# Optimization experiments

Hardware: AMD Instinct MI355X
Metric: run time of the kernel (lower is better)

The kernel has to match this reference:

```python
import jax, jax.numpy as jnp
import numpy as np

NUM_HEADS = 16
HEAD_DIM = 80
HIDDEN = 1280
SEQ = 3072
NUM_SEGS = 6  # 6 packed images of 512 patches each


def rotate_half(x):
    x1, x2 = jnp.split(x, 2, axis=-1)
    return jnp.concatenate([-x2, x1], axis=-1)


def setup_inputs() -> dict:
    key = jax.random.key(0)
    ks = jax.random.split(key, 6)
    hidden_states = jax.random.normal(ks[0], (SEQ, HIDDEN), dtype=jnp.float32)
    # RoPE tables as in Qwen-VL vision: freqs over half the head_dim, duplicated
    half = HEAD_DIM // 2
    inv_freq = 1.0 / (10000.0 ** (jnp.arange(half, dtype=jnp.float32) / half))
    pos = jnp.arange(SEQ, dtype=jnp.float32)[:, None]
    freqs = pos * inv_freq[None, :]                      # (SEQ, half)
    emb = jnp.concatenate([freqs, freqs], axis=-1)       # (SEQ, HEAD_DIM)
    cos = jnp.cos(emb)
    sin = jnp.sin(emb)
    # Packed segment boundaries: [0, 512, 1024, ..., 3072]
    cu_seqlens = jnp.arange(0, SEQ + 1, SEQ // NUM_SEGS, dtype=jnp.int32)
    scale = 0.02
    w_qkv = jax.random.normal(ks[1], (3 * HIDDEN, HIDDEN), dtype=jnp.float32) * scale
    b_qkv = jax.random.normal(ks[2], (3 * HIDDEN,), dtype=jnp.float32) * scale
    w_proj = jax.random.normal(ks[3], (HIDDEN, HIDDEN), dtype=jnp.float32) * scale
    b_proj = jax.random.normal(ks[4], (HIDDEN,), dtype=jnp.float32) * scale
    return {
        "hidden_states": hidden_states, "cos": cos, "sin": sin,
        "w_qkv": w_qkv, "b_qkv": b_qkv, "w_proj": w_proj, "b_proj": b_proj,
        "cu_seqlens": cu_seqlens,
    }


def reference(hidden_states, cos, sin, w_qkv, b_qkv, w_proj, b_proj, cu_seqlens):
    S, H = hidden_states.shape
    nh, hd = NUM_HEADS, H // NUM_HEADS

    # Fused QKV projection: (S, 3H) -> q, k, v each (S, nh, hd)
    qkv = hidden_states @ w_qkv.T + b_qkv
    qkv = qkv.reshape(S, 3, nh, hd)
    q, k, v = qkv[:, 0], qkv[:, 1], qkv[:, 2]

    # Inline RoPE on q/k (cos/sin broadcast over heads)
    c = cos[:, None, :]
    s = sin[:, None, :]
    q = q * c + rotate_half(q) * s
    k = k * c + rotate_half(k) * s

    # Original casts fp32 -> fp16 for the flash attention kernel
    q16 = q.astype(jnp.float16)
    k16 = k.astype(jnp.float16)
    v16 = v.astype(jnp.float16)

    # Varlen masking: tokens attend only within their own packed segment
    tok = jnp.arange(S)
    seg = jnp.searchsorted(cu_seqlens, tok, side="right")  # (S,)
    same_seg = seg[:, None] == seg[None, :]                 # (S, S)

    scale = hd ** (-0.5)
    # Scores accumulated in fp32 (as flash attention does internally)
    scores = jnp.einsum("qhd,khd->hqk", q16, k16,
                        preferred_element_type=jnp.float32) * scale
    scores = jnp.where(same_seg[None], scores, jnp.finfo(jnp.float32).min)
    weights = jax.nn.softmax(scores, axis=-1).astype(jnp.float16)  # (nh, S, S)

    attn = jnp.einsum("hqk,khd->qhd", weights, v16)  # (S, nh, hd) fp16
    attn = attn.astype(jnp.float32).reshape(S, H)
    return attn @ w_proj.T + b_proj
```

## Files before the change

kernel.cpp:

```cpp
#include <hip/hip_runtime.h>

typedef _Float16 f16;
typedef _Float16 half8 __attribute__((ext_vector_type(8)));
typedef _Float16 half4 __attribute__((ext_vector_type(4)));
typedef float f32x4 __attribute__((ext_vector_type(4)));

__device__ __forceinline__ void gld_lds16(const void* g, void* l) {
  __builtin_amdgcn_global_load_lds((const __attribute__((address_space(1))) void*)g,
                                   (__attribute__((address_space(3))) void*)l, 16, 0, 0);
}

template <int CTRL>
__device__ __forceinline__ float dppf(float x) {
  return __builtin_bit_cast(float,
      __builtin_amdgcn_mov_dpp(__builtin_bit_cast(int, x), CTRL, 0xf, 0xf, true));
}
__device__ __forceinline__ float dpp_max16(float v) {
  v = fmaxf(v, dppf<0xB1>(v));
  v = fmaxf(v, dppf<0x4E>(v));
  v = fmaxf(v, dppf<0x128>(v));
  v = fmaxf(v, dppf<0x140>(v));
  return v;
}
__device__ __forceinline__ float dpp_sum16(float v) {
  v += dppf<0xB1>(v);
  v += dppf<0x4E>(v);
  v += dppf<0x128>(v);
  v += dppf<0x140>(v);
  return v;
}

__global__ void cvt_all(const float* __restrict__ hid, const float* __restrict__ wq,
                        const float* __restrict__ wp, f16* __restrict__ hid16,
                        f16* __restrict__ wq16, f16* __restrict__ wp16) {
  int b = blockIdx.x;
  const float* in;
  f16* out;
  int i;
  if (b < 3840) { in = hid; out = hid16; i = b * 256 + threadIdx.x; }
  else if (b < 8640) { in = wq; out = wq16; i = (b - 3840) * 256 + threadIdx.x; }
  else { in = wp; out = wp16; i = (b - 8640) * 256 + threadIdx.x; }
  float4 v = ((const float4*)in)[i];
  half4 o;
  o.x = (f16)v.x; o.y = (f16)v.y; o.z = (f16)v.z; o.w = (f16)v.w;
  ((half4*)out)[i] = o;
}

__global__ __launch_bounds__(512, 2) void gemm256(const f16* __restrict__ A,
                                                  const f16* __restrict__ B,
                                                  const float* __restrict__ bias,
                                                  f16* __restrict__ C) {
  __shared__ f16 S[65536];
  char* Sb = (char*)S;
  const int tid = threadIdx.x, lane = tid & 63, wid = tid >> 6;
  const int lm = lane & 15, q4 = lane >> 4;
  const int wm = wid >> 2, wn = wid & 3;
  const int bm = blockIdx.x * 256, bn = blockIdx.y * 256;
  const int w2 = wid * 2048;

  const int ch = ((lane & 7) ^ (lane >> 3)) << 3;
  const int r0 = wid * 16 + (lane >> 3);
  const int r1 = r0 + 8;
  uint32_t aoff[2][2], boff[2][2];
#pragma unroll
  for (int h = 0; h < 2; h++) {
    aoff[h][0] = (uint32_t)((bm + h * 64 + (r0 & 63) + ((r0 >> 6) << 7)) * 1280 + ch);
    aoff[h][1] = (uint32_t)((bm + h * 64 + (r1 & 63) + ((r1 >> 6) << 7)) * 1280 + ch);
    boff[h][0] = (uint32_t)((bn + h * 32 + (r0 & 31) + ((r0 >> 5) << 6)) * 1280 + ch);
    boff[h][1] = (uint32_t)((bn + h * 32 + (r1 & 31) + ((r1 >> 5) << 6)) * 1280 + ch);
  }

  int aro[4][2], bro[2][2];
#pragma unroll
  for (int f = 0; f < 4; f++)
#pragma unroll
    for (int ks = 0; ks < 2; ks++) {
      int row = wm * 64 + f * 16 + lm, colb = ks * 64 + q4 * 16;
      aro[f][ks] = row * 128 + (colb ^ ((row & 7) << 4));
    }
#pragma unroll
  for (int j = 0; j < 2; j++)
#pragma unroll
    for (int ks = 0; ks < 2; ks++) {
      int row = wn * 32 + j * 16 + lm, colb = ks * 64 + q4 * 16;
      bro[j][ks] = row * 128 + (colb ^ ((row & 7) << 4));
    }

  f32x4 acc[8][4] = {};

  {
    char* A0 = Sb;
    char* B0 = Sb + 65536;
    char* A1 = Sb + 32768;
    char* B1 = Sb + 98304;
    gld_lds16(A + aoff[0][0], A0 + w2);
    gld_lds16(A + aoff[0][1], A0 + w2 + 1024);
    gld_lds16(B + boff[1][0], B0 + 16384 + w2);
    gld_lds16(B + boff[1][1], B0 + 16384 + w2 + 1024);
    gld_lds16(A + aoff[1][0], A0 + 16384 + w2);
    gld_lds16(A + aoff[1][1], A0 + 16384 + w2 + 1024);
    gld_lds16(B + boff[0][0], B0 + w2);
    gld_lds16(B + boff[0][1], B0 + w2 + 1024);
    gld_lds16(A + aoff[0][0] + 64, A1 + w2);
    gld_lds16(A + aoff[0][1] + 64, A1 + w2 + 1024);
    gld_lds16(B + boff[1][0] + 64, B1 + 16384 + w2);
    gld_lds16(B + boff[1][1] + 64, B1 + 16384 + w2 + 1024);
    gld_lds16(A + aoff[1][0] + 64, A1 + 16384 + w2);
    gld_lds16(A + aoff[1][1] + 64, A1 + 16384 + w2 + 1024);
    asm volatile("s_waitcnt vmcnt(6)" ::: "memory");
    __builtin_amdgcn_s_barrier();
  }

  constexpr int NT = 20;
  half8 af[4][2], bf[2][2];
  for (int t = 0; t < NT; ++t) {
    const int p = t & 1;
    char* Ab = Sb + p * 32768;
    char* Bb = Sb + 65536 + p * 32768;
    char* Bn = Sb + 65536 + (p ^ 1) * 32768;
    const int k1 = (t + 1 < NT ? t + 1 : NT - 1) * 64;
    const int k2 = (t + 2 < NT ? t + 2 : NT - 1) * 64;

#pragma unroll
    for (int f = 0; f < 4; f++) {
      af[f][0] = *(const half8*)(Ab + aro[f][0]);
      af[f][1] = *(const half8*)(Ab + aro[f][1]);
    }
#pragma unroll
    for (int j = 0; j < 2; j++) {
      bf[j][0] = *(const half8*)(Bb + bro[j][0]);
      bf[j][1] = *(const half8*)(Bb + bro[j][1]);
    }
    gld_lds16(B + boff[0][0] + k1, Bn + w2);
    gld_lds16(B + boff[0][1] + k1, Bn + w2 + 1024);
    __builtin_amdgcn_s_barrier();
    asm volatile("s_waitcnt lgkmcnt(0)" ::: "memory");
    __builtin_amdgcn_sched_barrier(0);
    __builtin_amdgcn_s_setprio(1);
#pragma unroll
    for (int ks = 0; ks < 2; ks++)
#pragma unroll
      for (int f = 0; f < 4; f++)
#pragma unroll
        for (int j = 0; j < 2; j++)
          acc[f][j] =
              __builtin_amdgcn_mfma_f32_16x16x32_f16(af[f][ks], bf[j][ks], acc[f][j], 0, 0, 0);
    __builtin_amdgcn_s_setprio(0);
    __builtin_amdgcn_s_barrier();

#pragma unroll
    for (int j = 0; j < 2; j++) {
      bf[j][0] = *(const half8*)(Bb + 16384 + bro[j][0]);
      bf[j][1] = *(const half8*)(Bb + 16384 + bro[j][1]);
    }
    gld_lds16(A + aoff[0][0] + k2, Ab + w2);
    gld_lds16(A + aoff[0][1] + k2, Ab + w2 + 1024);
    __builtin_amdgcn_s_barrier();
    asm volatile("s_waitcnt lgkmcnt(0)" ::: "memory");
    __builtin_amdgcn_sched_barrier(0);
    __builtin_amdgcn_s_setprio(1);
#pragma unroll
    for (int ks = 0; ks < 2; ks++)
#pragma unroll
      for (int f = 0; f < 4; f++)
#pragma unroll
        for (int j = 0; j < 2; j++)
          acc[f][2 + j] =
              __builtin_amdgcn_mfma_f32_16x16x32_f16(af[f][ks], bf[j][ks], acc[f][2 + j], 0, 0, 0);
    __builtin_amdgcn_s_setprio(0);
    __builtin_amdgcn_s_barrier();

#pragma unroll
    for (int f = 0; f < 4; f++) {
      af[f][0] = *(const half8*)(Ab + 16384 + aro[f][0]);
      af[f][1] = *(const half8*)(Ab + 16384 + aro[f][1]);
    }
    gld_lds16(B + boff[1][0] + k2, Bb + 16384 + w2);
    gld_lds16(B + boff[1][1] + k2, Bb + 16384 + w2 + 1024);
    __builtin_amdgcn_s_barrier();
    asm volatile("s_waitcnt lgkmcnt(0)" ::: "memory");
    __builtin_amdgcn_sched_barrier(0);
    __builtin_amdgcn_s_setprio(1);
#pragma unroll
    for (int ks = 0; ks < 2; ks++)
#pragma unroll
      for (int f = 0; f < 4; f++)
#pragma unroll
        for (int j = 0; j < 2; j++)
          acc[4 + f][2 + j] = __builtin_amdgcn_mfma_f32_16x16x32_f16(af[f][ks], bf[j][ks],
                                                                     acc[4 + f][2 + j], 0, 0, 0);
    __builtin_amdgcn_s_setprio(0);
    __builtin_amdgcn_s_barrier();

#pragma unroll
    for (int j = 0; j < 2; j++) {
      bf[j][0] = *(const half8*)(Bb + bro[j][0]);
      bf[j][1] = *(const half8*)(Bb + bro[j][1]);
    }
    gld_lds16(A + aoff[1][0] + k2, Ab + 16384 + w2);
    gld_lds16(A + aoff[1][1] + k2, Ab + 16384 + w2 + 1024);
    asm volatile("s_waitcnt vmcnt(6)" ::: "memory");
    __builtin_amdgcn_s_barrier();
    asm volatile("s_waitcnt lgkmcnt(0)" ::: "memory");
    __builtin_amdgcn_sched_barrier(0);
    __builtin_amdgcn_s_setprio(1);
#pragma unroll
    for (int ks = 0; ks < 2; ks++)
#pragma unroll
      for (int f = 0; f < 4; f++)
#pragma unroll
        for (int j = 0; j < 2; j++)
          acc[4 + f][j] =
              __builtin_amdgcn_mfma_f32_16x16x32_f16(af[f][ks], bf[j][ks], acc[4 + f][j], 0, 0, 0);
    __builtin_amdgcn_s_setprio(0);
    __builtin_amdgcn_s_barrier();
  }

#pragma unroll
  for (int mf = 0; mf < 8; mf++)
#pragma unroll
    for (int nf = 0; nf < 4; nf++) {
      const int gc = bn + wn * 64 + nf * 16 + lm;
      const float bb = bias[gc];
      const int gr0 = bm + wm * 128 + mf * 16 + q4 * 4;
#pragma unroll
      for (int r = 0; r < 4; r++)
        C[(size_t)(gr0 + r) * 3840 + gc] = (f16)(acc[mf][nf][r] + bb);
    }
}

template <bool OUT_F16>
__global__ __launch_bounds__(256, 2) void gemm_bt64(const f16* __restrict__ A,
                                                    const f16* __restrict__ B,
                                                    const float* __restrict__ bias,
                                                    void* __restrict__ Cout,
                                                    int K, int lda, int ldb, int ldc) {
  __shared__ f16 As[64 * 32];
  __shared__ f16 Bs[128 * 32];
  const int tid = threadIdx.x, lane = tid & 63, wave = tid >> 6;
  const int bm = blockIdx.x * 64, bn = blockIdx.y * 128;
  const int wm = (wave & 1) * 32, wn = (wave >> 1) * 64;
  const int lm = lane & 15, kq = (lane >> 4) * 8;
  const int arow = tid >> 2, acol = (tid & 3) * 8;

  const f16* Ab = A + (size_t)(bm + arow) * lda + acol;
  const f16* Bb = B + (size_t)(bn + arow) * ldb + acol;
  f16* AsW = As + wave * 512;
  f16* BsW = Bs + wave * 512;

  f32x4 acc[2][4] = {};
  for (int k0 = 0; k0 < K; k0 += 32) {
    gld_lds16(Ab + k0, AsW);
    gld_lds16(Bb + k0, BsW);
    gld_lds16(Bb + (size_t)64 * ldb + k0, BsW + 2048);
    __syncthreads();
    half8 af[2], bf[4];
#pragma unroll
    for (int mt = 0; mt < 2; mt++) af[mt] = *(const half8*)&As[(wm + 16 * mt + lm) * 32 + kq];
#pragma unroll
    for (int nt = 0; nt < 4; nt++) bf[nt] = *(const half8*)&Bs[(wn + 16 * nt + lm) * 32 + kq];
#pragma unroll
    for (int mt = 0; mt < 2; mt++)
#pragma unroll
      for (int nt = 0; nt < 4; nt++)
        acc[mt][nt] = __builtin_amdgcn_mfma_f32_16x16x32_f16(af[mt], bf[nt], acc[mt][nt], 0, 0, 0);
    __syncthreads();
  }
  const int q4 = lane >> 4;
#pragma unroll
  for (int mt = 0; mt < 2; mt++)
#pragma unroll
    for (int nt = 0; nt < 4; nt++)
#pragma unroll
      for (int r = 0; r < 4; r++) {
        int gr = bm + wm + 16 * mt + 4 * q4 + r;
        int gc = bn + wn + 16 * nt + lm;
        float v = acc[mt][nt][r] + bias[gc];
        if (OUT_F16)
          ((f16*)Cout)[(size_t)gr * ldc + gc] = (f16)v;
        else
          ((float*)Cout)[(size_t)gr * ldc + gc] = v;
      }
}

__global__ void rope_transpose(f16* __restrict__ qkv, const float* __restrict__ cosb,
                               const float* __restrict__ sinb, f16* __restrict__ vt) {
  __shared__ f16 tile[64][72];
  const int b = blockIdx.x;
  if (b < 1920) {
    int idx = b * 256 + threadIdx.x;
    int c = idx % 5;
    int t = idx / 5;
    int h = t % 16; t /= 16;
    int qk = t & 1;
    int s = t >> 1;
    size_t base = (size_t)s * 3840 + qk * 1280 + h * 80 + c * 8;
    half8 x = *(half8*)&qkv[base];
    half8 y = *(half8*)&qkv[base + 40];
    const float* cp = cosb + s * 80 + c * 8;
    const float* sp = sinb + s * 80 + c * 8;
    half8 ox, oy;
#pragma unroll
    for (int i = 0; i < 8; i++) {
      float cs = cp[i], sn = sp[i];
      float xf = (float)x[i], yf = (float)y[i];
      ox[i] = (f16)(xf * cs - yf * sn);
      oy[i] = (f16)(yf * cs + xf * sn);
    }
    *(half8*)&qkv[base] = ox;
    *(half8*)&qkv[base + 40] = oy;
  } else {
    const int bb = b - 1920;
    const int bs = (bb % 48) * 64;
    const int bd = (bb / 48) * 64;
    const int r = threadIdx.x >> 2, c = (threadIdx.x & 3) * 16;
    *(uint4*)&tile[r][c] = *(const uint4*)&qkv[(size_t)(bs + r) * 3840 + 2560 + bd + c];
    *(uint4*)&tile[r][c + 8] = *(const uint4*)&qkv[(size_t)(bs + r) * 3840 + 2560 + bd + c + 8];
    __syncthreads();
    f16 tmp[16];
#pragma unroll
    for (int i = 0; i < 16; i++) tmp[i] = tile[c + i][r];
    *(uint4*)&vt[(size_t)(bd + r) * 3072 + bs + c] = *(uint4*)&tmp[0];
    *(uint4*)&vt[(size_t)(bd + r) * 3072 + bs + c + 8] = *(uint4*)&tmp[8];
  }
}

__global__ __launch_bounds__(256, 3) void flash_attn6(const f16* __restrict__ qkv,
                                                      const f16* __restrict__ vt,
                                                      f16* __restrict__ attn) {
  __shared__ f16 S[25088];
  const int tid = threadIdx.x, lane = tid & 63, wave = tid >> 6;
  const int lm = lane & 15, q4 = lane >> 4;
  const int h = blockIdx.x, g = blockIdx.z;
  const int qbase = g * 512 + blockIdx.y * 64 + wave * 16;
  f16* P = S + 20480 + wave * 1152;
  const half8 hz = {};

  const f16* qrow = qkv + (size_t)(qbase + lm) * 3840 + h * 80;
  half8 qf[3];
  qf[0] = *(const half8*)(qrow + q4 * 8);
  qf[1] = *(const half8*)(qrow + 32 + q4 * 8);
  qf[2] = (q4 < 2) ? *(const half8*)(qrow + 64 + q4 * 8) : hz;

  const bool isK = wave < 2;
  const f16* gsrc = isK ? qkv : vt;
  const uint32_t gstep = isK ? (uint32_t)(64 * 3840) : 64u;
  const int cbase = (wave & 1) * 5;
  const uint32_t ldsoff = (isK ? 0u : 5120u) + (uint32_t)cbase * 512u;
  uint32_t goff[5];
#pragma unroll
  for (int i = 0; i < 5; i++) {
    int t = (cbase + i) * 1024 + lane * 16;
    if (isK) {
      int row = t / 160, colb = t % 160;
      goff[i] = (uint32_t)((g * 512 + row) * 3840 + 1280 + h * 80 + (colb >> 1));
    } else {
      int vd = t >> 7, vsb = t & 127;
      int vsrc = vsb ^ ((vd & 7) << 4);
      goff[i] = (uint32_t)((h * 80 + vd) * 3072 + g * 512 + (vsrc >> 1));
    }
  }

  f32x4 oacc[5] = {};
  float mprev[4] = {-1e30f, -1e30f, -1e30f, -1e30f};
  float lsum[4] = {0.f, 0.f, 0.f, 0.f};
  const float sc = 0.11180339887498949f * 1.4426950408889634f;

#pragma unroll
  for (int i = 0; i < 5; i++) gld_lds16(gsrc + goff[i], S + ldsoff + i * 512);
  __syncthreads();

  for (int jj = 0; jj < 8; jj++) {
    const int p = jj & 1;
    f16* Kb = S + p * 10240;
    f16* Vb = Kb + 5120;
    if (jj < 7) {
#pragma unroll
      for (int i = 0; i < 5; i++)
        gld_lds16(gsrc + goff[i] + (uint32_t)(jj + 1) * gstep,
                  S + (p ^ 1) * 10240 + ldsoff + i * 512);
    }

    f32x4 sacc[4] = {};
#pragma unroll
    for (int ks = 0; ks < 3; ks++) {
      half8 bk[4];
#pragma unroll
      for (int nt = 0; nt < 4; nt++)
        bk[nt] = (ks < 2 || q4 < 2)
                     ? *(const half8*)&Kb[(16 * nt + lm) * 80 + 32 * ks + q4 * 8]
                     : hz;
#pragma unroll
      for (int nt = 0; nt < 4; nt++)
        sacc[nt] = __builtin_amdgcn_mfma_f32_16x16x32_f16(qf[ks], bk[nt], sacc[nt], 0, 0, 0);
    }

    float mnew[4], alpha[4], rs[4];
#pragma unroll
    for (int r = 0; r < 4; r++) {
      float v = fmaxf(fmaxf(sacc[0][r], sacc[1][r]), fmaxf(sacc[2][r], sacc[3][r]));
      v = dpp_max16(v);
      mnew[r] = fmaxf(mprev[r], v * sc);
      alpha[r] = __builtin_exp2f(mprev[r] - mnew[r]);
      mprev[r] = mnew[r];
      rs[r] = 0.f;
    }
#pragma unroll
    for (int nt = 0; nt < 4; nt++)
#pragma unroll
      for (int r = 0; r < 4; r++) {
        float pp = __builtin_exp2f(sacc[nt][r] * sc - mnew[r]);
        sacc[nt][r] = pp;
        rs[r] += pp;
      }
#pragma unroll
    for (int r = 0; r < 4; r++) {
      float v = dpp_sum16(rs[r]);
      lsum[r] = alpha[r] * lsum[r] + v;
#pragma unroll
      for (int nt2 = 0; nt2 < 5; nt2++) oacc[nt2][r] *= alpha[r];
    }

#pragma unroll
    for (int nt = 0; nt < 4; nt++)
#pragma unroll
      for (int r = 0; r < 4; r++)
        P[(4 * q4 + r) * 72 + 16 * nt + lm] = (f16)sacc[nt][r];

#pragma unroll
    for (int ks = 0; ks < 2; ks++) {
      half8 ap = *(const half8*)&P[lm * 72 + ks * 32 + q4 * 8];
      half8 bv[5];
#pragma unroll
      for (int nt2 = 0; nt2 < 5; nt2++) {
        int row = 16 * nt2 + lm;
        bv[nt2] = *(const half8*)&Vb[row * 64 + ((ks * 32 + q4 * 8) ^ ((row & 7) << 3))];
      }
#pragma unroll
      for (int nt2 = 0; nt2 < 5; nt2++)
        oacc[nt2] = __builtin_amdgcn_mfma_f32_16x16x32_f16(ap, bv[nt2], oacc[nt2], 0, 0, 0);
    }

    __syncthreads();
  }

#pragma unroll
  for (int r = 0; r < 4; r++) {
    float inv = 1.0f / lsum[r];
    int s = qbase + 4 * q4 + r;
#pragma unroll
    for (int nt2 = 0; nt2 < 5; nt2++)
      attn[(size_t)s * 1280 + h * 80 + 16 * nt2 + lm] = (f16)(oacc[nt2][r] * inv);
  }
}

extern "C" void kernel_launch(void* const* d_in, const int* in_sizes, int n_in,
                              void* d_out, int out_size, void* d_ws, size_t ws_size,
                              hipStream_t stream) {
  const float* hidden = (const float*)d_in[0];
  const float* cosb   = (const float*)d_in[1];
  const float* sinb   = (const float*)d_in[2];
  const float* w_qkv  = (const float*)d_in[3];
  const float* b_qkv  = (const float*)d_in[4];
  const float* w_proj = (const float*)d_in[5];
  const float* b_proj = (const float*)d_in[6];

  char* ws = (char*)d_ws;
  f16* hidden16 = (f16*)(ws + 0);
  f16* wqkv16   = (f16*)(ws + 7864320);
  f16* wproj16  = (f16*)(ws + 17694720);
  f16* qkv16    = (f16*)(ws + 20971520);
  f16* attn16   = (f16*)(ws + 44564480);
  f16* vt16     = hidden16;

  cvt_all<<<10240, 256, 0, stream>>>(hidden, w_qkv, w_proj, hidden16, wqkv16, wproj16);

  gemm256<<<dim3(12, 15), 512, 0, stream>>>(hidden16, wqkv16, b_qkv, qkv16);

  rope_transpose<<<2880, 256, 0, stream>>>(qkv16, cosb, sinb, vt16);

  flash_attn6<<<dim3(16, 8, 6), 256, 0, stream>>>(qkv16, vt16, attn16);

  gemm_bt64<false><<<dim3(48, 10), 256, 0, stream>>>(attn16, wproj16, b_proj, d_out,
                                                     1280, 1280, 1280, 1280);
}
```

Measured before the change: 194.3 us.

## Retile QKV GEMM to 256x192 blocks over 240 workgroups with swizzled mapping

Replaces the 256x256-tile QKV GEMM (180 blocks) with 256x192 tiles, giving 240 blocks so the grid fills more of the MI355X compute units. It adds a block-index swizzle to improve L2 locality and reworks the LDS layout, warp fragment mapping and the pipelined load schedule to match the new tile shape. The trade-off is a smaller tile with lower arithmetic intensity per block, plus a more intricate load/barrier schedule that could expose latency.

```diff
diff --git a/kernel.cpp b/kernel.cpp
--- a/kernel.cpp
+++ b/kernel.cpp
@@ -46,93 +46,79 @@
   ((half4*)out)[i] = o;
 }
 
-__global__ __launch_bounds__(512, 2) void gemm256(const f16* __restrict__ A,
+__global__ __launch_bounds__(512, 2) void gemm240(const f16* __restrict__ A,
                                                   const f16* __restrict__ B,
                                                   const float* __restrict__ bias,
                                                   f16* __restrict__ C) {
-  __shared__ f16 S[65536];
+  __shared__ f16 S[57344];
   char* Sb = (char*)S;
   const int tid = threadIdx.x, lane = tid & 63, wid = tid >> 6;
   const int lm = lane & 15, q4 = lane >> 4;
   const int wm = wid >> 2, wn = wid & 3;
-  const int bm = blockIdx.x * 256, bn = blockIdx.y * 256;
-  const int w2 = wid * 2048;
+  const int swz = ((int)blockIdx.x & 7) * 30 + ((int)blockIdx.x >> 3);
+  const int bm = (swz % 12) * 256, bn = (swz / 12) * 192;
 
   const int ch = ((lane & 7) ^ (lane >> 3)) << 3;
-  const int r0 = wid * 16 + (lane >> 3);
-  const int r1 = r0 + 8;
-  uint32_t aoff[2][2], boff[2][2];
-#pragma unroll
-  for (int h = 0; h < 2; h++) {
-    aoff[h][0] = (uint32_t)((bm + h * 64 + (r0 & 63) + ((r0 >> 6) << 7)) * 1280 + ch);
-    aoff[h][1] = (uint32_t)((bm + h * 64 + (r1 & 63) + ((r1 >> 6) << 7)) * 1280 + ch);
-    boff[h][0] = (uint32_t)((bn + h * 32 + (r0 & 31) + ((r0 >> 5) << 6)) * 1280 + ch);
-    boff[h][1] = (uint32_t)((bn + h * 32 + (r1 & 31) + ((r1 >> 5) << 6)) * 1280 + ch);
-  }
-
-  int aro[4][2], bro[2][2];
-#pragma unroll
-  for (int f = 0; f < 4; f++)
-#pragma unroll
-    for (int ks = 0; ks < 2; ks++) {
-      int row = wm * 64 + f * 16 + lm, colb = ks * 64 + q4 * 16;
-      aro[f][ks] = row * 128 + (colb ^ ((row & 7) << 4));
-    }
-#pragma unroll
-  for (int j = 0; j < 2; j++)
-#pragma unroll
-    for (int ks = 0; ks < 2; ks++) {
-      int row = wn * 32 + j * 16 + lm, colb = ks * 64 + q4 * 16;
-      bro[j][ks] = row * 128 + (colb ^ ((row & 7) << 4));
-    }
-
-  f32x4 acc[8][4] = {};
+  uint32_t aoff[4], boff[3];
+#pragma unroll
+  for (int q = 0; q < 4; q++)
+    aoff[q] = (uint32_t)((bm + q * 64 + wid * 8 + (lane >> 3)) * 1280 + ch);
+#pragma unroll
+  for (int i = 0; i < 3; i++)
+    boff[i] = (uint32_t)((bn + wid * 24 + i * 8 + (lane >> 3)) * 1280 + ch);
+
+  const int xr = (lm & 7) << 4;
+  int aro[2][2], bro[3][2];
+#pragma unroll
+  for (int f = 0; f < 2; f++)
+#pragma unroll
+    for (int ks = 0; ks < 2; ks++)
+      aro[f][ks] = (wm * 32 + f * 16 + lm) * 128 + ((ks * 64 + q4 * 16) ^ xr);
+#pragma unroll
+  for (int nh = 0; nh < 3; nh++)
+#pragma unroll
+    for (int ks = 0; ks < 2; ks++)
+      bro[nh][ks] = (nh * 64 + wn * 16 + lm) * 128 + ((ks * 64 + q4 * 16) ^ xr);
+
+  f32x4 acc[8][3] = {};
 
   {
-    char* A0 = Sb;
-    char* B0 = Sb + 65536;
-    char* A1 = Sb + 32768;
-    char* B1 = Sb + 98304;
-    gld_lds16(A + aoff[0][0], A0 + w2);
-    gld_lds16(A + aoff[0][1], A0 + w2 + 1024);
-    gld_lds16(B + boff[1][0], B0 + 16384 + w2);
-    gld_lds16(B + boff[1][1], B0 + 16384 + w2 + 1024);
-    gld_lds16(A + aoff[1][0], A0 + 16384 + w2);
-    gld_lds16(A + aoff[1][1], A0 + 16384 + w2 + 1024);
-    gld_lds16(B + boff[0][0], B0 + w2);
-    gld_lds16(B + boff[0][1], B0 + w2 + 1024);
-    gld_lds16(A + aoff[0][0] + 64, A1 + w2);
-    gld_lds16(A + aoff[0][1] + 64, A1 + w2 + 1024);
-    gld_lds16(B + boff[1][0] + 64, B1 + 16384 + w2);
-    gld_lds16(B + boff[1][1] + 64, B1 + 16384 + w2 + 1024);
-    gld_lds16(A + aoff[1][0] + 64, A1 + 16384 + w2);
-    gld_lds16(A + aoff[1][1] + 64, A1 + 16384 + w2 + 1024);
+#pragma unroll
+    for (int q = 0; q < 4; q++)
+      gld_lds16(A + aoff[q], Sb + q * 8192 + wid * 1024);
+#pragma unroll
+    for (int i = 0; i < 3; i++)
+      gld_lds16(B + boff[i], Sb + 65536 + (3 * wid + i) * 1024);
+#pragma unroll
+    for (int i = 0; i < 3; i++)
+      gld_lds16(B + boff[i] + 64, Sb + 65536 + 24576 + (3 * wid + i) * 1024);
+#pragma unroll
+    for (int q = 0; q < 3; q++)
+      gld_lds16(A + aoff[q] + 64, Sb + 32768 + q * 8192 + wid * 1024);
     asm volatile("s_waitcnt vmcnt(6)" ::: "memory");
     __builtin_amdgcn_s_barrier();
   }
 
   constexpr int NT = 20;
-  half8 af[4][2], bf[2][2];
+  half8 af[2][2], bf[3][2];
   for (int t = 0; t < NT; ++t) {
     const int p = t & 1;
     char* Ab = Sb + p * 32768;
-    char* Bb = Sb + 65536 + p * 32768;
-    char* Bn = Sb + 65536 + (p ^ 1) * 32768;
+    char* Bb = Sb + 65536 + p * 24576;
     const int k1 = (t + 1 < NT ? t + 1 : NT - 1) * 64;
     const int k2 = (t + 2 < NT ? t + 2 : NT - 1) * 64;
 
 #pragma unroll
-    for (int f = 0; f < 4; f++) {
+    for (int f = 0; f < 2; f++) {
       af[f][0] = *(const half8*)(Ab + aro[f][0]);
       af[f][1] = *(const half8*)(Ab + aro[f][1]);
     }
 #pragma unroll
-    for (int j = 0; j < 2; j++) {
-      bf[j][0] = *(const half8*)(Bb + bro[j][0]);
-      bf[j][1] = *(const half8*)(Bb + bro[j][1]);
-    }
-    gld_lds16(B + boff[0][0] + k1, Bn + w2);
-    gld_lds16(B + boff[0][1] + k1, Bn + w2 + 1024);
+    for (int nh = 0; nh < 3; nh++) {
+      bf[nh][0] = *(const half8*)(Bb + bro[nh][0]);
+      bf[nh][1] = *(const half8*)(Bb + bro[nh][1]);
+    }
+    gld_lds16(A + aoff[3] + k1, Sb + (p ^ 1) * 32768 + 3 * 8192 + wid * 1024);
     __builtin_amdgcn_s_barrier();
     asm volatile("s_waitcnt lgkmcnt(0)" ::: "memory");
     __builtin_amdgcn_sched_barrier(0);
@@ -140,21 +126,23 @@
 #pragma unroll
     for (int ks = 0; ks < 2; ks++)
 #pragma unroll
-      for (int f = 0; f < 4; f++)
-#pragma unroll
-        for (int j = 0; j < 2; j++)
-          acc[f][j] =
-              __builtin_amdgcn_mfma_f32_16x16x32_f16(af[f][ks], bf[j][ks], acc[f][j], 0, 0, 0);
+      for (int f = 0; f < 2; f++)
+#pragma unroll
+        for (int nh = 0; nh < 3; nh++)
+          acc[f][nh] =
+              __builtin_amdgcn_mfma_f32_16x16x32_f16(af[f][ks], bf[nh][ks], acc[f][nh], 0, 0, 0);
     __builtin_amdgcn_s_setprio(0);
     __builtin_amdgcn_s_barrier();
 
 #pragma unroll
-    for (int j = 0; j < 2; j++) {
-      bf[j][0] = *(const half8*)(Bb + 16384 + bro[j][0]);
-      bf[j][1] = *(const half8*)(Bb + 16384 + bro[j][1]);
-    }
-    gld_lds16(A + aoff[0][0] + k2, Ab + w2);
-    gld_lds16(A + aoff[0][1] + k2, Ab + w2 + 1024);
+    for (int f = 0; f < 2; f++) {
+      af[f][0] = *(const half8*)(Ab + 8192 + aro[f][0]);
+      af[f][1] = *(const half8*)(Ab + 8192 + aro[f][1]);
+    }
+#pragma unroll
+    for (int i = 0; i < 3; i++)
+      gld_lds16(B + boff[i] + k2, Bb + (3 * wid + i) * 1024);
+    gld_lds16(A + aoff[0] + k2, Ab + wid * 1024);
     __builtin_amdgcn_s_barrier();
     asm volatile("s_waitcnt lgkmcnt(0)" ::: "memory");
     __builtin_amdgcn_sched_barrier(0);
@@ -162,21 +150,20 @@
 #pragma unroll
     for (int ks = 0; ks < 2; ks++)
 #pragma unroll
-      for (int f = 0; f < 4; f++)
-#pragma unroll
-        for (int j = 0; j < 2; j++)
-          acc[f][2 + j] =
-              __builtin_amdgcn_mfma_f32_16x16x32_f16(af[f][ks], bf[j][ks], acc[f][2 + j], 0, 0, 0);
+      for (int f = 0; f < 2; f++)
+#pragma unroll
+        for (int nh = 0; nh < 3; nh++)
+          acc[2 + f][nh] = __builtin_amdgcn_mfma_f32_16x16x32_f16(af[f][ks], bf[nh][ks],
+                                                                  acc[2 + f][nh], 0, 0, 0);
     __builtin_amdgcn_s_setprio(0);
     __builtin_amdgcn_s_barrier();
 
 #pragma unroll
-    for (int f = 0; f < 4; f++) {
+    for (int f = 0; f < 2; f++) {
       af[f][0] = *(const half8*)(Ab + 16384 + aro[f][0]);
       af[f][1] = *(const half8*)(Ab + 16384 + aro[f][1]);
     }
-    gld_lds16(B + boff[1][0] + k2, Bb + 16384 + w2);
-    gld_lds16(B + boff[1][1] + k2, Bb + 16384 + w2 + 1024);
+    gld_lds16(A + aoff[1] + k2, Ab + 8192 + wid * 1024);
     __builtin_amdgcn_s_barrier();
     asm volatile("s_waitcnt lgkmcnt(0)" ::: "memory");
     __builtin_amdgcn_sched_barrier(0);
@@ -184,21 +171,20 @@
 #pragma unroll
     for (int ks = 0; ks < 2; ks++)
 #pragma unroll
-      for (int f = 0; f < 4; f++)
-#pragma unroll
-        for (int j = 0; j < 2; j++)
-          acc[4 + f][2 + j] = __builtin_amdgcn_mfma_f32_16x16x32_f16(af[f][ks], bf[j][ks],
-                                                                     acc[4 + f][2 + j], 0, 0, 0);
+      for (int f = 0; f < 2; f++)
+#pragma unroll
+        for (int nh = 0; nh < 3; nh++)
+          acc[4 + f][nh] = __builtin_amdgcn_mfma_f32_16x16x32_f16(af[f][ks], bf[nh][ks],
+                                                                  acc[4 + f][nh], 0, 0, 0);
     __builtin_amdgcn_s_setprio(0);
     __builtin_amdgcn_s_barrier();
 
 #pragma unroll
-    for (int j = 0; j < 2; j++) {
-      bf[j][0] = *(const half8*)(Bb + bro[j][0]);
-      bf[j][1] = *(const half8*)(Bb + bro[j][1]);
-    }
-    gld_lds16(A + aoff[1][0] + k2, Ab + 16384 + w2);
-    gld_lds16(A + aoff[1][1] + k2, Ab + 16384 + w2 + 1024);
+    for (int f = 0; f < 2; f++) {
+      af[f][0] = *(const half8*)(Ab + 24576 + aro[f][0]);
+      af[f][1] = *(const half8*)(Ab + 24576 + aro[f][1]);
+    }
+    gld_lds16(A + aoff[2] + k2, Ab + 16384 + wid * 1024);
     asm volatile("s_waitcnt vmcnt(6)" ::: "memory");
     __builtin_amdgcn_s_barrier();
     asm volatile("s_waitcnt lgkmcnt(0)" ::: "memory");
@@ -207,11 +193,11 @@
 #pragma unroll
     for (int ks = 0; ks < 2; ks++)
 #pragma unroll
-      for (int f = 0; f < 4; f++)
-#pragma unroll
-        for (int j = 0; j < 2; j++)
-          acc[4 + f][j] =
-              __builtin_amdgcn_mfma_f32_16x16x32_f16(af[f][ks], bf[j][ks], acc[4 + f][j], 0, 0, 0);
+      for (int f = 0; f < 2; f++)
+#pragma unroll
+        for (int nh = 0; nh < 3; nh++)
+          acc[6 + f][nh] = __builtin_amdgcn_mfma_f32_16x16x32_f16(af[f][ks], bf[nh][ks],
+                                                                  acc[6 + f][nh], 0, 0, 0);
     __builtin_amdgcn_s_setprio(0);
     __builtin_amdgcn_s_barrier();
   }
@@ -219,10 +205,10 @@
 #pragma unroll
   for (int mf = 0; mf < 8; mf++)
 #pragma unroll
-    for (int nf = 0; nf < 4; nf++) {
-      const int gc = bn + wn * 64 + nf * 16 + lm;
+    for (int nf = 0; nf < 3; nf++) {
+      const int gc = bn + nf * 64 + wn * 16 + lm;
       const float bb = bias[gc];
-      const int gr0 = bm + wm * 128 + mf * 16 + q4 * 4;
+      const int gr0 = bm + (mf >> 1) * 64 + wm * 32 + (mf & 1) * 16 + q4 * 4;
 #pragma unroll
       for (int r = 0; r < 4; r++)
         C[(size_t)(gr0 + r) * 3840 + gc] = (f16)(acc[mf][nf][r] + bb);
@@ -475,7 +461,7 @@
 
   cvt_all<<<10240, 256, 0, stream>>>(hidden, w_qkv, w_proj, hidden16, wqkv16, wproj16);
 
-  gemm256<<<dim3(12, 15), 512, 0, stream>>>(hidden16, wqkv16, b_qkv, qkv16);
+  gemm240<<<240, 512, 0, stream>>>(hidden16, wqkv16, b_qkv, qkv16);
 
   rope_transpose<<<2880, 256, 0, stream>>>(qkv16, cosb, sinb, vt16);
 
```

Result: faster. 189.3 us (-2.5%).
